# Kernel optimization log

Hardware: AMD Instinct MI355X
Metric: run time of the kernel (lower is better)

Reference implementation:

```python
import jax, jax.numpy as jnp
import numpy as np

B, S, V, H = 256, 512, 768, 50


def setup_inputs() -> dict:
    key = jax.random.key(0)
    ks = jax.random.split(key, 5)
    sc = 1.0 / np.sqrt(V)
    return {
        "output_1": jax.random.normal(ks[0], (B, S, V), dtype=jnp.float32),
        "output_2": jax.random.normal(ks[1], (B, S, V), dtype=jnp.float32),
        "Wg": jax.random.normal(ks[2], (H, 2 * V), dtype=jnp.float32) * sc,
        "bg": jnp.zeros((H,), dtype=jnp.float32),
        "Wfd": jax.random.normal(ks[3], (H, 2 * H), dtype=jnp.float32) * 0.1,
        "bfd": jnp.zeros((H,), dtype=jnp.float32),
        "Wff": jax.random.normal(ks[4], (1, H), dtype=jnp.float32) * 0.1,
        "bff": jnp.zeros((1,), dtype=jnp.float32),
    }


def reference(output_1, output_2, Wg, bg, Wfd, bfd, Wff, bff):
    # Append doc-mean sentence: [B, S+1, V]
    x1 = jnp.concatenate([output_1, jnp.mean(output_1, axis=1, keepdims=True)], axis=1)
    x2 = jnp.concatenate([output_2, jnp.mean(output_2, axis=1, keepdims=True)], axis=1)

    # Bidirectional cross-attention scores: a[b, s, t] = <x1[b,s], x2[b,t]>
    a = jnp.einsum('bsv,btv->bst', x1, x2)
    a_x = jax.nn.softmax(a, axis=1)   # softmax over x1's sentence axis
    a_y = jax.nn.softmax(a, axis=0)   # softmax over the BATCH axis (as in the original)

    attention_x = jnp.einsum('bst,bsv->btv', a_x, x1)  # [B, S+1, V]
    attention_y = jnp.einsum('bst,btv->bsv', a_y, x2)  # [B, S+1, V]

    out_x = jnp.concatenate([x1, attention_y], axis=2) @ Wg.T + bg  # [B, S+1, H]
    out_y = jnp.concatenate([x2, attention_x], axis=2) @ Wg.T + bg

    # Training branch: take the doc-mean (last) position
    o1 = out_x[:, -1, :]  # [B, H]
    o2 = out_y[:, -1, :]
    h = jax.nn.relu(jnp.concatenate([o1, o2], axis=1) @ Wfd.T + bfd)  # [B, H]
    logit = jnp.squeeze(h @ Wff.T + bff)  # [B]
    return jax.nn.sigmoid(logit)
```

## Files before the change

kernel.cpp:

```cpp
#include <hip/hip_runtime.h>
#include <math.h>

#define BB 256
#define SS 512
#define VV 768
#define TT 513
#define HH 50

#define OFF_M1    0
#define OFF_M2    (OFF_M1 + BB*VV)
#define OFF_XPART (OFF_M2 + BB*VV)
#define XPART_STRIDE 772
#define OFF_AROW  (OFF_XPART + 4*BB*XPART_STRIDE)
#define AROW_STRIDE 520
#define OFF_COLM  (OFF_AROW + BB*AROW_STRIDE)
#define OFF_COLRD (OFF_COLM + 520)
#define OFF_YPART (OFF_COLRD + 520)

__global__ __launch_bounds__(192) void k_mean(const float* __restrict__ o1,
                                              const float* __restrict__ o2,
                                              float* __restrict__ ws) {
    int bid   = blockIdx.x;
    int chunk = bid & 3;
    int b     = (bid >> 2) & (BB - 1);
    int tensor = bid >> 10;
    const float* src = tensor ? o2 : o1;
    float* dst = ws + (tensor ? OFF_M2 : OFF_M1) + b * VV;
    int tid = threadIdx.x;
    const float4* p = (const float4*)(src + (size_t)b * SS * VV + (size_t)chunk * 128 * VV) + tid;
    float4 acc = {0.f, 0.f, 0.f, 0.f};
#pragma unroll 4
    for (int s = 0; s < 128; ++s) {
        float4 x = p[(size_t)s * 192];
        acc.x += x.x; acc.y += x.y; acc.z += x.z; acc.w += x.w;
    }
    const float inv = 1.0f / 512.0f;
    float* d4 = dst + tid * 4;
    atomicAdd(d4 + 0, acc.x * inv);
    atomicAdd(d4 + 1, acc.y * inv);
    atomicAdd(d4 + 2, acc.z * inv);
    atomicAdd(d4 + 3, acc.w * inv);
}

#define XCHUNK 8
__global__ __launch_bounds__(256) void k_xside(const float* __restrict__ o1,
                                               float* __restrict__ ws) {
    int part = blockIdx.x & 3;
    int b    = blockIdx.x >> 2;
    int tid  = threadIdx.x;
    int wave = tid >> 6, lane = tid & 63;
    __shared__ __align__(16) float m2s[VV];
    __shared__ __align__(16) float tile[XCHUNK][VV];
    __shared__ float sc[XCHUNK];

    const float* m2p = ws + OFF_M2 + b * VV;
    for (int i = tid; i < VV; i += 256) m2s[i] = m2p[i];
    __syncthreads();

    float accv[3] = {0.f, 0.f, 0.f};
    float M = -1e30f, d = 0.f;
    int s0 = part * 128;
    const float* base = o1 + (size_t)b * SS * VV;

    for (int c = 0; c < 128 / XCHUNK; ++c) {
        const float4* g = (const float4*)(base + (size_t)(s0 + c * XCHUNK) * VV);
        float4* l4 = (float4*)&tile[0][0];
#pragma unroll
        for (int k = 0; k < 6; ++k) l4[k * 256 + tid] = g[k * 256 + tid];
        __syncthreads();
#pragma unroll
        for (int r2 = 0; r2 < 2; ++r2) {
            int r = wave * 2 + r2;
            float p = 0.f;
#pragma unroll
            for (int k = 0; k < 12; ++k) p += tile[r][lane + 64 * k] * m2s[lane + 64 * k];
#pragma unroll
            for (int off = 32; off > 0; off >>= 1) p += __shfl_down(p, off);
            if (lane == 0) sc[r] = p;
        }
        __syncthreads();
        float sv[XCHUNK], cmax = -1e30f;
#pragma unroll
        for (int j = 0; j < XCHUNK; ++j) { sv[j] = sc[j]; cmax = fmaxf(cmax, sv[j]); }
        float newM  = fmaxf(M, cmax);
        float scale = __expf(M - newM);
        float w[XCHUNK], wsum = 0.f;
#pragma unroll
        for (int j = 0; j < XCHUNK; ++j) { w[j] = __expf(sv[j] - newM); wsum += w[j]; }
        d = d * scale + wsum;
#pragma unroll
        for (int i = 0; i < 3; ++i) {
            int v = tid + 256 * i;
            float a = accv[i] * scale;
#pragma unroll
            for (int j = 0; j < XCHUNK; ++j) a += w[j] * tile[j][v];
            accv[i] = a;
        }
        M = newM;
        __syncthreads();
    }

    if (part == 3) {
        const float* m1p = ws + OFF_M1 + b * VV;
        for (int i = tid; i < VV; i += 256) tile[0][i] = m1p[i];
        __syncthreads();
        if (wave == 0) {
            float p = 0.f;
#pragma unroll
            for (int k = 0; k < 12; ++k) p += tile[0][lane + 64 * k] * m2s[lane + 64 * k];
#pragma unroll
            for (int off = 32; off > 0; off >>= 1) p += __shfl_down(p, off);
            if (lane == 0) sc[0] = p;
        }
        __syncthreads();
        float s0v   = sc[0];
        float newM  = fmaxf(M, s0v);
        float scale = __expf(M - newM);
        float w0    = __expf(s0v - newM);
        d = d * scale + w0;
#pragma unroll
        for (int i = 0; i < 3; ++i) {
            int v = tid + 256 * i;
            accv[i] = accv[i] * scale + w0 * tile[0][v];
        }
        M = newM;
    }

    float* outp = ws + OFF_XPART + (size_t)(part * BB + b) * XPART_STRIDE;
#pragma unroll
    for (int i = 0; i < 3; ++i) outp[tid + 256 * i] = accv[i];
    if (tid == 0) { outp[768] = M; outp[769] = d; }
}

__global__ __launch_bounds__(256) void k_yscore(const float* __restrict__ o2,
                                                float* __restrict__ ws) {
    int bid = blockIdx.x;
    int tc = bid & 7, b = bid >> 3;
    int wave = threadIdx.x >> 6, lane = threadIdx.x & 63;
    const float4* m14 = (const float4*)(ws + OFF_M1 + b * VV);
    float4 mf[3];
#pragma unroll
    for (int k = 0; k < 3; ++k) mf[k] = m14[lane + 64 * k];
    const float* base = o2 + (size_t)b * SS * VV;
    float* arow = ws + OFF_AROW + b * AROW_STRIDE;
    for (int i = 0; i < 16; ++i) {
        int t = tc * 64 + wave * 16 + i;
        const float4* r4 = (const float4*)(base + (size_t)t * VV);
        float p = 0.f;
#pragma unroll
        for (int k = 0; k < 3; ++k) {
            float4 x = r4[lane + 64 * k];
            p += x.x * mf[k].x + x.y * mf[k].y + x.z * mf[k].z + x.w * mf[k].w;
        }
#pragma unroll
        for (int off = 32; off > 0; off >>= 1) p += __shfl_down(p, off);
        if (lane == 0) arow[t] = p;
    }
    if (tc == 7 && wave == 0) {
        const float4* r4 = (const float4*)(ws + OFF_M2 + b * VV);
        float p = 0.f;
#pragma unroll
        for (int k = 0; k < 3; ++k) {
            float4 x = r4[lane + 64 * k];
            p += x.x * mf[k].x + x.y * mf[k].y + x.z * mf[k].z + x.w * mf[k].w;
        }
#pragma unroll
        for (int off = 32; off > 0; off >>= 1) p += __shfl_down(p, off);
        if (lane == 0) arow[SS] = p;
    }
}

__global__ __launch_bounds__(256) void k_colstats(float* __restrict__ ws) {
    int t = blockIdx.x;
    int tid = threadIdx.x;
    int wave = tid >> 6, lane = tid & 63;
    float v = ws[OFF_AROW + tid * AROW_STRIDE + t];
    __shared__ float red[4], red2[4];
    float m = v;
#pragma unroll
    for (int off = 32; off > 0; off >>= 1) m = fmaxf(m, __shfl_down(m, off));
    if (lane == 0) red[wave] = m;
    __syncthreads();
    float m0 = fmaxf(fmaxf(red[0], red[1]), fmaxf(red[2], red[3]));
    float e = __expf(v - m0);
#pragma unroll
    for (int off = 32; off > 0; off >>= 1) e += __shfl_down(e, off);
    if (lane == 0) red2[wave] = e;
    __syncthreads();
    if (tid == 0) {
        float D = red2[0] + red2[1] + red2[2] + red2[3];
        ws[OFF_COLM + t]  = m0;
        ws[OFF_COLRD + t] = 1.0f / D;
    }
}

__global__ __launch_bounds__(192) void k_yweight(const float* __restrict__ o2,
                                                 float* __restrict__ ws) {
    int part = blockIdx.x & 3, b = blockIdx.x >> 2;
    int tid = threadIdx.x;
    __shared__ float wl[129];
    int t0 = part * 128;
    const float* arow = ws + OFF_AROW + b * AROW_STRIDE;
    for (int i = tid; i < 129; i += 192) {
        if (i < 128) {
            int t = t0 + i;
            wl[i] = __expf(arow[t] - ws[OFF_COLM + t]) * ws[OFF_COLRD + t];
        } else if (part == 3) {
            wl[128] = __expf(arow[SS] - ws[OFF_COLM + SS]) * ws[OFF_COLRD + SS];
        }
    }
    __syncthreads();
    const float4* base = (const float4*)(o2 + (size_t)b * SS * VV) + tid;
    float4 acc = {0.f, 0.f, 0.f, 0.f};
    for (int i = 0; i < 128; ++i) {
        float w = wl[i];
        float4 x = base[(size_t)(t0 + i) * 192];
        acc.x += w * x.x; acc.y += w * x.y; acc.z += w * x.z; acc.w += w * x.w;
    }
    if (part == 3) {
        float w = wl[128];
        float4 x = ((const float4*)(ws + OFF_M2 + b * VV))[tid];
        acc.x += w * x.x; acc.y += w * x.y; acc.z += w * x.z; acc.w += w * x.w;
    }
    ((float4*)(ws + OFF_YPART + (size_t)(part * BB + b) * VV))[tid] = acc;
}

__global__ __launch_bounds__(256) void k_epilogue(const float* __restrict__ Wg,
                                                  const float* __restrict__ bg,
                                                  const float* __restrict__ Wfd,
                                                  const float* __restrict__ bfd,
                                                  const float* __restrict__ Wff,
                                                  const float* __restrict__ bff,
                                                  float* __restrict__ ws,
                                                  float* __restrict__ out) {
    int b = blockIdx.x;
    int tid = threadIdx.x;
    __shared__ __align__(16) float cx[2 * VV];
    __shared__ __align__(16) float cy[2 * VV];
    __shared__ float od[2][HH][2];
    __shared__ float o1s[HH], o2s[HH];

    float Mp[4], dp[4];
#pragma unroll
    for (int p = 0; p < 4; ++p) {
        const float* xp = ws + OFF_XPART + (size_t)(p * BB + b) * XPART_STRIDE;
        Mp[p] = xp[768];
        dp[p] = xp[769];
    }
    float M = fmaxf(fmaxf(Mp[0], Mp[1]), fmaxf(Mp[2], Mp[3]));
    float e[4], den = 0.f;
#pragma unroll
    for (int p = 0; p < 4; ++p) { e[p] = __expf(Mp[p] - M); den += dp[p] * e[p]; }
    float rden = 1.0f / den;

    for (int i = tid; i < VV; i += 256) {
        cx[i] = ws[OFF_M1 + b * VV + i];
        cy[i] = ws[OFF_M2 + b * VV + i];
        float ay = 0.f;
#pragma unroll
        for (int p = 0; p < 4; ++p) ay += ws[OFF_YPART + (size_t)(p * BB + b) * VV + i];
        cx[VV + i] = ay;
        float ax = 0.f;
#pragma unroll
        for (int p = 0; p < 4; ++p) ax += ws[OFF_XPART + (size_t)(p * BB + b) * XPART_STRIDE + i] * e[p];
        cy[VV + i] = ax * rden;
    }
    __syncthreads();

    if (tid < 200) {
        int which = tid / 100, r = tid % 100, h = r >> 1, seg = r & 1;
        const float* c = which ? cy : cx;
        const float4* cc = (const float4*)(c + seg * VV);
        const float4* wg = (const float4*)(Wg + (size_t)h * 2 * VV + seg * VV);
        float acc = 0.f;
        for (int j = 0; j < VV / 4; ++j) {
            float4 a4 = cc[j]; float4 w4 = wg[j];
            acc += a4.x * w4.x + a4.y * w4.y + a4.z * w4.z + a4.w * w4.w;
        }
        od[which][h][seg] = acc;
    }
    __syncthreads();
    if (tid < HH)                     o1s[tid]      = od[0][tid][0]    + od[0][tid][1]    + bg[tid];
    else if (tid >= 64 && tid < 64 + HH) { int h = tid - 64; o2s[h] = od[1][h][0] + od[1][h][1] + bg[h]; }
    __syncthreads();
    if (tid < 64) {
        float hv = 0.f;
        if (tid < HH) {
            float a = bfd[tid];
            for (int k = 0; k < HH; ++k)
                a += o1s[k] * Wfd[tid * 2 * HH + k] + o2s[k] * Wfd[tid * 2 * HH + HH + k];
            hv = fmaxf(a, 0.f) * Wff[tid];
        }
#pragma unroll
        for (int off = 32; off > 0; off >>= 1) hv += __shfl_down(hv, off);
        if (tid == 0) out[b] = 1.0f / (1.0f + __expf(-(hv + bff[0])));
    }
}

extern "C" void kernel_launch(void* const* d_in, const int* in_sizes, int n_in,
                              void* d_out, int out_size, void* d_ws, size_t ws_size,
                              hipStream_t stream) {
    const float* o1  = (const float*)d_in[0];
    const float* o2  = (const float*)d_in[1];
    const float* Wg  = (const float*)d_in[2];
    const float* bg  = (const float*)d_in[3];
    const float* Wfd = (const float*)d_in[4];
    const float* bfd = (const float*)d_in[5];
    const float* Wff = (const float*)d_in[6];
    const float* bff = (const float*)d_in[7];
    float* out = (float*)d_out;
    float* ws  = (float*)d_ws;

    hipMemsetAsync(ws, 0, (size_t)2 * BB * VV * sizeof(float), stream);

    k_mean    <<<2048, 192, 0, stream>>>(o1, o2, ws);
    k_xside   <<<1024, 256, 0, stream>>>(o1, ws);
    k_yscore  <<<2048, 256, 0, stream>>>(o2, ws);
    k_colstats<<< 513, 256, 0, stream>>>(ws);
    k_yweight <<<1024, 192, 0, stream>>>(o2, ws);
    k_epilogue<<< 256, 256, 0, stream>>>(Wg, bg, Wfd, bfd, Wff, bff, ws, out);
}
```

Baseline: 1.003 ms.

## Fuse output_2 mean into y-score pass and reorder kernels for cache reuse

Computes the doc-mean of output_2 inside the y-score kernel while it already streams output_2, removing one full read of that tensor. The mean-mean score moves into colstats and the epilogue folds the extra x-side softmax term. k_xside now runs last and double-buffers its tile through registers to overlap global loads with compute. k_yweight traverses batches in reverse so it reads the output_2 data most recently touched by the preceding pass, which may still be in cache. The trade-off is more atomics and shared-memory reduction in the fused kernel, plus extra register pressure in xside.

```diff
diff --git a/kernel.cpp b/kernel.cpp
--- a/kernel.cpp
+++ b/kernel.cpp
@@ -17,17 +17,14 @@
 #define OFF_COLRD (OFF_COLM + 520)
 #define OFF_YPART (OFF_COLRD + 520)
 
-__global__ __launch_bounds__(192) void k_mean(const float* __restrict__ o1,
-                                              const float* __restrict__ o2,
-                                              float* __restrict__ ws) {
+__global__ __launch_bounds__(192) void k_mean1(const float* __restrict__ o1,
+                                               float* __restrict__ ws) {
     int bid   = blockIdx.x;
     int chunk = bid & 3;
-    int b     = (bid >> 2) & (BB - 1);
-    int tensor = bid >> 10;
-    const float* src = tensor ? o2 : o1;
-    float* dst = ws + (tensor ? OFF_M2 : OFF_M1) + b * VV;
+    int b     = bid >> 2;
+    float* dst = ws + OFF_M1 + b * VV;
     int tid = threadIdx.x;
-    const float4* p = (const float4*)(src + (size_t)b * SS * VV + (size_t)chunk * 128 * VV) + tid;
+    const float4* p = (const float4*)(o1 + (size_t)b * SS * VV + (size_t)chunk * 128 * VV) + tid;
     float4 acc = {0.f, 0.f, 0.f, 0.f};
 #pragma unroll 4
     for (int s = 0; s < 128; ++s) {
@@ -42,131 +39,47 @@
     atomicAdd(d4 + 3, acc.w * inv);
 }
 
-#define XCHUNK 8
-__global__ __launch_bounds__(256) void k_xside(const float* __restrict__ o1,
-                                               float* __restrict__ ws) {
-    int part = blockIdx.x & 3;
-    int b    = blockIdx.x >> 2;
-    int tid  = threadIdx.x;
-    int wave = tid >> 6, lane = tid & 63;
-    __shared__ __align__(16) float m2s[VV];
-    __shared__ __align__(16) float tile[XCHUNK][VV];
-    __shared__ float sc[XCHUNK];
-
-    const float* m2p = ws + OFF_M2 + b * VV;
-    for (int i = tid; i < VV; i += 256) m2s[i] = m2p[i];
-    __syncthreads();
-
-    float accv[3] = {0.f, 0.f, 0.f};
-    float M = -1e30f, d = 0.f;
-    int s0 = part * 128;
-    const float* base = o1 + (size_t)b * SS * VV;
-
-    for (int c = 0; c < 128 / XCHUNK; ++c) {
-        const float4* g = (const float4*)(base + (size_t)(s0 + c * XCHUNK) * VV);
-        float4* l4 = (float4*)&tile[0][0];
-#pragma unroll
-        for (int k = 0; k < 6; ++k) l4[k * 256 + tid] = g[k * 256 + tid];
-        __syncthreads();
-#pragma unroll
-        for (int r2 = 0; r2 < 2; ++r2) {
-            int r = wave * 2 + r2;
-            float p = 0.f;
-#pragma unroll
-            for (int k = 0; k < 12; ++k) p += tile[r][lane + 64 * k] * m2s[lane + 64 * k];
-#pragma unroll
-            for (int off = 32; off > 0; off >>= 1) p += __shfl_down(p, off);
-            if (lane == 0) sc[r] = p;
-        }
-        __syncthreads();
-        float sv[XCHUNK], cmax = -1e30f;
-#pragma unroll
-        for (int j = 0; j < XCHUNK; ++j) { sv[j] = sc[j]; cmax = fmaxf(cmax, sv[j]); }
-        float newM  = fmaxf(M, cmax);
-        float scale = __expf(M - newM);
-        float w[XCHUNK], wsum = 0.f;
-#pragma unroll
-        for (int j = 0; j < XCHUNK; ++j) { w[j] = __expf(sv[j] - newM); wsum += w[j]; }
-        d = d * scale + wsum;
-#pragma unroll
-        for (int i = 0; i < 3; ++i) {
-            int v = tid + 256 * i;
-            float a = accv[i] * scale;
-#pragma unroll
-            for (int j = 0; j < XCHUNK; ++j) a += w[j] * tile[j][v];
-            accv[i] = a;
-        }
-        M = newM;
-        __syncthreads();
-    }
-
-    if (part == 3) {
-        const float* m1p = ws + OFF_M1 + b * VV;
-        for (int i = tid; i < VV; i += 256) tile[0][i] = m1p[i];
-        __syncthreads();
-        if (wave == 0) {
-            float p = 0.f;
-#pragma unroll
-            for (int k = 0; k < 12; ++k) p += tile[0][lane + 64 * k] * m2s[lane + 64 * k];
-#pragma unroll
-            for (int off = 32; off > 0; off >>= 1) p += __shfl_down(p, off);
-            if (lane == 0) sc[0] = p;
-        }
-        __syncthreads();
-        float s0v   = sc[0];
-        float newM  = fmaxf(M, s0v);
-        float scale = __expf(M - newM);
-        float w0    = __expf(s0v - newM);
-        d = d * scale + w0;
-#pragma unroll
-        for (int i = 0; i < 3; ++i) {
-            int v = tid + 256 * i;
-            accv[i] = accv[i] * scale + w0 * tile[0][v];
-        }
-        M = newM;
-    }
-
-    float* outp = ws + OFF_XPART + (size_t)(part * BB + b) * XPART_STRIDE;
-#pragma unroll
-    for (int i = 0; i < 3; ++i) outp[tid + 256 * i] = accv[i];
-    if (tid == 0) { outp[768] = M; outp[769] = d; }
-}
-
-__global__ __launch_bounds__(256) void k_yscore(const float* __restrict__ o2,
-                                                float* __restrict__ ws) {
-    int bid = blockIdx.x;
-    int tc = bid & 7, b = bid >> 3;
-    int wave = threadIdx.x >> 6, lane = threadIdx.x & 63;
+__global__ __launch_bounds__(256) void k_m2yscore(const float* __restrict__ o2,
+                                                  float* __restrict__ ws) {
+    int tc = blockIdx.x & 3;
+    int b  = blockIdx.x >> 2;
+    int tid = threadIdx.x, wave = tid >> 6, lane = tid & 63;
+    __shared__ __align__(16) float msum[4][VV];
+
     const float4* m14 = (const float4*)(ws + OFF_M1 + b * VV);
     float4 mf[3];
 #pragma unroll
     for (int k = 0; k < 3; ++k) mf[k] = m14[lane + 64 * k];
+
     const float* base = o2 + (size_t)b * SS * VV;
     float* arow = ws + OFF_AROW + b * AROW_STRIDE;
-    for (int i = 0; i < 16; ++i) {
-        int t = tc * 64 + wave * 16 + i;
+    float4 acc[3];
+#pragma unroll
+    for (int k = 0; k < 3; ++k) acc[k] = make_float4(0.f, 0.f, 0.f, 0.f);
+
+    int t0 = tc * 128 + wave * 32;
+    for (int i = 0; i < 32; ++i) {
+        int t = t0 + i;
         const float4* r4 = (const float4*)(base + (size_t)t * VV);
         float p = 0.f;
 #pragma unroll
         for (int k = 0; k < 3; ++k) {
             float4 x = r4[lane + 64 * k];
+            acc[k].x += x.x; acc[k].y += x.y; acc[k].z += x.z; acc[k].w += x.w;
             p += x.x * mf[k].x + x.y * mf[k].y + x.z * mf[k].z + x.w * mf[k].w;
         }
 #pragma unroll
         for (int off = 32; off > 0; off >>= 1) p += __shfl_down(p, off);
         if (lane == 0) arow[t] = p;
     }
-    if (tc == 7 && wave == 0) {
-        const float4* r4 = (const float4*)(ws + OFF_M2 + b * VV);
-        float p = 0.f;
-#pragma unroll
-        for (int k = 0; k < 3; ++k) {
-            float4 x = r4[lane + 64 * k];
-            p += x.x * mf[k].x + x.y * mf[k].y + x.z * mf[k].z + x.w * mf[k].w;
-        }
-#pragma unroll
-        for (int off = 32; off > 0; off >>= 1) p += __shfl_down(p, off);
-        if (lane == 0) arow[SS] = p;
+    float4* ms4 = (float4*)msum[wave];
+#pragma unroll
+    for (int k = 0; k < 3; ++k) ms4[lane + 64 * k] = acc[k];
+    __syncthreads();
+    const float inv = 1.0f / 512.0f;
+    for (int i = tid; i < VV; i += 256) {
+        float s = msum[0][i] + msum[1][i] + msum[2][i] + msum[3][i];
+        atomicAdd(ws + OFF_M2 + b * VV + i, s * inv);
     }
 }
 
@@ -174,7 +87,21 @@
     int t = blockIdx.x;
     int tid = threadIdx.x;
     int wave = tid >> 6, lane = tid & 63;
-    float v = ws[OFF_AROW + tid * AROW_STRIDE + t];
+    float v;
+    if (t == SS) {
+        const float4* a = (const float4*)(ws + OFF_M1 + tid * VV);
+        const float4* c = (const float4*)(ws + OFF_M2 + tid * VV);
+        float p = 0.f;
+#pragma unroll 8
+        for (int k = 0; k < VV / 4; ++k) {
+            float4 x = a[k], y = c[k];
+            p += x.x * y.x + x.y * y.y + x.z * y.z + x.w * y.w;
+        }
+        v = p;
+        ws[OFF_AROW + tid * AROW_STRIDE + SS] = v;
+    } else {
+        v = ws[OFF_AROW + tid * AROW_STRIDE + t];
+    }
     __shared__ float red[4], red2[4];
     float m = v;
 #pragma unroll
@@ -196,7 +123,7 @@
 
 __global__ __launch_bounds__(192) void k_yweight(const float* __restrict__ o2,
                                                  float* __restrict__ ws) {
-    int part = blockIdx.x & 3, b = blockIdx.x >> 2;
+    int part = blockIdx.x & 3, b = (BB - 1) - (blockIdx.x >> 2);
     int tid = threadIdx.x;
     __shared__ float wl[129];
     int t0 = part * 128;
@@ -223,6 +150,86 @@
         acc.x += w * x.x; acc.y += w * x.y; acc.z += w * x.z; acc.w += w * x.w;
     }
     ((float4*)(ws + OFF_YPART + (size_t)(part * BB + b) * VV))[tid] = acc;
+}
+
+#define XCHUNK 8
+__global__ __launch_bounds__(256) void k_xside(const float* __restrict__ o1,
+                                               float* __restrict__ ws) {
+    int part = blockIdx.x & 3;
+    int b    = blockIdx.x >> 2;
+    int tid  = threadIdx.x;
+    int wave = tid >> 6, lane = tid & 63;
+    __shared__ __align__(16) float m2s[VV];
+    __shared__ __align__(16) float tile[2][XCHUNK][VV];
+    __shared__ float sc[XCHUNK];
+
+    const float* m2p = ws + OFF_M2 + b * VV;
+    for (int i = tid; i < VV; i += 256) m2s[i] = m2p[i];
+
+    float accv[3] = {0.f, 0.f, 0.f};
+    float M = -1e30f, d = 0.f;
+    int s0 = part * 128;
+    const float* base = o1 + (size_t)b * SS * VV;
+
+    float4 r[6];
+    {
+        const float4* g = (const float4*)(base + (size_t)s0 * VV);
+#pragma unroll
+        for (int k = 0; k < 6; ++k) r[k] = g[k * 256 + tid];
+        float4* l4 = (float4*)&tile[0][0][0];
+#pragma unroll
+        for (int k = 0; k < 6; ++k) l4[k * 256 + tid] = r[k];
+    }
+    __syncthreads();
+
+    for (int c = 0; c < 128 / XCHUNK; ++c) {
+        int cur = c & 1;
+        if (c < 15) {
+            const float4* g = (const float4*)(base + (size_t)(s0 + (c + 1) * XCHUNK) * VV);
+#pragma unroll
+            for (int k = 0; k < 6; ++k) r[k] = g[k * 256 + tid];
+        }
+#pragma unroll
+        for (int r2 = 0; r2 < 2; ++r2) {
+            int rr = wave * 2 + r2;
+            float p = 0.f;
+#pragma unroll
+            for (int k = 0; k < 12; ++k) p += tile[cur][rr][lane + 64 * k] * m2s[lane + 64 * k];
+#pragma unroll
+            for (int off = 32; off > 0; off >>= 1) p += __shfl_down(p, off);
+            if (lane == 0) sc[rr] = p;
+        }
+        __syncthreads();
+        float sv[XCHUNK], cmax = -1e30f;
+#pragma unroll
+        for (int j = 0; j < XCHUNK; ++j) { sv[j] = sc[j]; cmax = fmaxf(cmax, sv[j]); }
+        float newM  = fmaxf(M, cmax);
+        float scale = __expf(M - newM);
+        float w[XCHUNK], wsum = 0.f;
+#pragma unroll
+        for (int j = 0; j < XCHUNK; ++j) { w[j] = __expf(sv[j] - newM); wsum += w[j]; }
+        d = d * scale + wsum;
+#pragma unroll
+        for (int i = 0; i < 3; ++i) {
+            int v = tid + 256 * i;
+            float a = accv[i] * scale;
+#pragma unroll
+            for (int j = 0; j < XCHUNK; ++j) a += w[j] * tile[cur][j][v];
+            accv[i] = a;
+        }
+        M = newM;
+        if (c < 15) {
+            float4* l4 = (float4*)&tile[1 - cur][0][0];
+#pragma unroll
+            for (int k = 0; k < 6; ++k) l4[k * 256 + tid] = r[k];
+        }
+        __syncthreads();
+    }
+
+    float* outp = ws + OFF_XPART + (size_t)(part * BB + b) * XPART_STRIDE;
+#pragma unroll
+    for (int i = 0; i < 3; ++i) outp[tid + 256 * i] = accv[i];
+    if (tid == 0) { outp[768] = M; outp[769] = d; }
 }
 
 __global__ __launch_bounds__(256) void k_epilogue(const float* __restrict__ Wg,
@@ -247,20 +254,25 @@
         Mp[p] = xp[768];
         dp[p] = xp[769];
     }
+    float sv = ws[OFF_AROW + b * AROW_STRIDE + SS];
     float M = fmaxf(fmaxf(Mp[0], Mp[1]), fmaxf(Mp[2], Mp[3]));
+    M = fmaxf(M, sv);
     float e[4], den = 0.f;
 #pragma unroll
     for (int p = 0; p < 4; ++p) { e[p] = __expf(Mp[p] - M); den += dp[p] * e[p]; }
+    float w0 = __expf(sv - M);
+    den += w0;
     float rden = 1.0f / den;
 
     for (int i = tid; i < VV; i += 256) {
-        cx[i] = ws[OFF_M1 + b * VV + i];
+        float m1v = ws[OFF_M1 + b * VV + i];
+        cx[i] = m1v;
         cy[i] = ws[OFF_M2 + b * VV + i];
         float ay = 0.f;
 #pragma unroll
         for (int p = 0; p < 4; ++p) ay += ws[OFF_YPART + (size_t)(p * BB + b) * VV + i];
         cx[VV + i] = ay;
-        float ax = 0.f;
+        float ax = w0 * m1v;
 #pragma unroll
         for (int p = 0; p < 4; ++p) ax += ws[OFF_XPART + (size_t)(p * BB + b) * XPART_STRIDE + i] * e[p];
         cy[VV + i] = ax * rden;
@@ -268,7 +280,7 @@
     __syncthreads();
 
     if (tid < 200) {
-        int which = tid / 100, r = tid % 100, h = r >> 1, seg = r & 1;
+        int which = tid / 100, rr = tid % 100, h = rr >> 1, seg = rr & 1;
         const float* c = which ? cy : cx;
         const float4* cc = (const float4*)(c + seg * VV);
         const float4* wg = (const float4*)(Wg + (size_t)h * 2 * VV + seg * VV);
@@ -313,10 +325,10 @@
 
     hipMemsetAsync(ws, 0, (size_t)2 * BB * VV * sizeof(float), stream);
 
-    k_mean    <<<2048, 192, 0, stream>>>(o1, o2, ws);
-    k_xside   <<<1024, 256, 0, stream>>>(o1, ws);
-    k_yscore  <<<2048, 256, 0, stream>>>(o2, ws);
+    k_mean1   <<<1024, 192, 0, stream>>>(o1, ws);
+    k_m2yscore<<<1024, 256, 0, stream>>>(o2, ws);
     k_colstats<<< 513, 256, 0, stream>>>(ws);
     k_yweight <<<1024, 192, 0, stream>>>(o2, ws);
+    k_xside   <<<1024, 256, 0, stream>>>(o1, ws);
     k_epilogue<<< 256, 256, 0, stream>>>(Wg, bg, Wfd, bfd, Wff, bff, ws, out);
 }
```

Result: slower. 1.058 ms (+5.5%).
